# Performance work log

Measured on AMD Instinct MI355X. Metric: run time of the kernel, lower is better.

## Reference

```python
import jax, jax.numpy as jnp
import numpy as np

B, S, A = 65536, 376, 17
H1, H2, K = 400, 300, 15
MAX_ACTION = 1.0


def setup_inputs() -> dict:
    key = jax.random.key(0)
    ks = jax.random.split(key, 16)

    def lin(kw, fan_in, fan_out):
        lim = 1.0 / np.sqrt(fan_in)
        k1, k2 = jax.random.split(kw)
        W = jax.random.uniform(k1, (fan_in, fan_out), jnp.float32, -lim, lim)
        b = jax.random.uniform(k2, (fan_out,), jnp.float32, -lim, lim)
        return W, b

    W1, b1 = lin(ks[0], S, H1)
    W2, b2 = lin(ks[1], H1, H2)
    Wmu, bmu = lin(ks[2], H2, A)
    Wlv, blv = lin(ks[3], H2, A)
    Wu, bu = lin(ks[4], H2, K * A)
    Ww, bw = lin(ks[5], H2, K * A)
    Wb, bb = lin(ks[6], H2, K)
    x = jax.random.normal(ks[7], (B, S), jnp.float32)
    eps = jax.random.normal(ks[8], (B, A), jnp.float32)
    return dict(x=x, eps=eps, W1=W1, b1=b1, W2=W2, b2=b2, Wmu=Wmu, bmu=bmu,
                Wlv=Wlv, blv=blv, Wu=Wu, bu=bu, Ww=Ww, bw=bw, Wb=Wb, bb=bb)


def _flow_chain(action, u, w, b):
    # u, w: (K, B, A); b: (K, B). Sequential planar flow -> lax.scan over K.
    def step(carry, uwb):
        z, ldj = carry
        u_k, w_k, b_k = uwb
        uw = jnp.sum(w_k * u_k, -1)                       # (B,)
        m_uw = -1.0 + jax.nn.softplus(uw)
        w_norm_sq = jnp.sum(w_k * w_k, -1)
        u_hat = u_k + ((m_uw - uw) / w_norm_sq)[:, None] * w_k  # invertibility reparam
        wzb = jnp.sum(w_k * z, -1) + b_k                  # (B,)
        t = jnp.tanh(wzb)
        z_new = z + u_hat * t[:, None]
        psi_u = jnp.sum(w_k * u_hat, -1) * (1.0 - t * t)  # psi^T u_hat
        ldj_new = ldj + jnp.log(jnp.abs(1.0 + psi_u))
        return (z_new, ldj_new), None

    init = (action, jnp.zeros(action.shape[0], action.dtype))
    (z_fin, ldj), _ = jax.lax.scan(step, init, (u, w, b))
    return z_fin, ldj


def reference(x, eps, W1, b1, W2, b2, Wmu, bmu, Wlv, blv, Wu, bu, Ww, bw, Wb, bb):
    h = jax.nn.relu(x @ W1 + b1)
    h = jax.nn.relu(h @ W2 + b2)
    mu = MAX_ACTION * jnp.tanh(h @ Wmu + bmu)
    log_var = MAX_ACTION * jnp.tanh(h @ Wlv + blv)
    std = jnp.exp(log_var)                 # torch code uses log_var.exp() as the scale
    action = mu + std * eps                # rsample

    u = (h @ Wu + bu).reshape(B, K, A).transpose(1, 0, 2)   # (K, B, A)
    w = (h @ Ww + bw).reshape(B, K, A).transpose(1, 0, 2)   # (K, B, A)
    b = (h @ Wb + bb).T                                      # (K, B)

    final_action, log_det_j = _flow_chain(action, u, w, b)

    # Normal(mu, std).log_prob(action) summed over action dim; (action-mu)/std == eps
    log_2pi = jnp.float32(np.log(2.0 * np.pi))
    log_prob = jnp.sum(-0.5 * eps * eps - log_var - 0.5 * log_2pi, axis=-1)
    log_prob_final = log_prob - log_det_j
    prob_final = jnp.exp(log_prob_final)
    return final_action, prob_final, log_prob_final
```

## Files before the change

### kernel.cpp

```cpp
#include <hip/hip_runtime.h>

typedef unsigned short ushort_t;
typedef unsigned int uint_t;
typedef __bf16 bf16x8 __attribute__((ext_vector_type(8)));
typedef float f32x4 __attribute__((ext_vector_type(4)));

#define B_ROWS 65536

#define KT1 12
#define NT1 30
#define KTC1 15
#define KI2 13
#define NT2 20
#define KTC2 10
#define KI3 10
#define NT3 50
#define KTH 25


#define SZ1 (NT1 * KT1 * 512)
#define SZ2 (NT2 * KI2 * 512)
#define SZ3 (NT3 * KI3 * 512)

#define H2_US  ((size_t)4096 * KTC2 * 512)
#define HEADS_US ((size_t)4096 * KTH * 512)

__device__ inline ushort_t f2bf(float f) {
    uint_t u = __float_as_uint(f);
    return (ushort_t)((u + 0x7FFFu + ((u >> 16) & 1u)) >> 16);
}
__device__ inline uint_t pack2(float a, float b) {
    return (uint_t)f2bf(a) | ((uint_t)f2bf(b) << 16);
}
__device__ inline float fast_tanh(float x) {
    float e = __expf(2.f * x);
    return 1.f - 2.f / (e + 1.f);
}
__device__ inline void gl2lds16(const ushort_t* g, ushort_t* l) {
    __builtin_amdgcn_global_load_lds(
        (const __attribute__((address_space(1))) uint_t*)g,
        (__attribute__((address_space(3))) uint_t*)l, 16, 0, 0);
}
__device__ inline void unpack8(uint4 v, float* dst) {
    uint_t q[4] = {v.x, v.y, v.z, v.w};
    #pragma unroll
    for (int m = 0; m < 4; ++m) {
        dst[2 * m]     = __uint_as_float(q[m] << 16);
        dst[2 * m + 1] = __uint_as_float(q[m] & 0xFFFF0000u);
    }
}

__global__ void pack_kernel(const float* __restrict__ W1, const float* __restrict__ W2,
                            const float* __restrict__ Wmu, const float* __restrict__ Wlv,
                            const float* __restrict__ Wu, const float* __restrict__ Ww,
                            const float* __restrict__ Wb,
                            const float* __restrict__ b1, const float* __restrict__ b2,
                            const float* __restrict__ bmu, const float* __restrict__ blv,
                            const float* __restrict__ bu, const float* __restrict__ bw,
                            const float* __restrict__ bb,
                            ushort_t* __restrict__ W1t, ushort_t* __restrict__ W2t,
                            ushort_t* __restrict__ Wht,
                            float* __restrict__ b1p, float* __restrict__ b2p,
                            float* __restrict__ bHp)
{
    int i = blockIdx.x * 256 + threadIdx.x;
    if (i < SZ1) {
        int t = i >> 9, pos = i & 511;
        int l = pos >> 3, j = pos & 7;
        int n = (t / KT1) * 16 + (l & 15);
        int k = (t % KT1) * 32 + (l >> 4) * 8 + j;
        W1t[i] = (n < 400 && k < 376) ? f2bf(W1[k * 400 + n]) : (ushort_t)0;
    } else if (i < SZ1 + SZ2) {
        int i2 = i - SZ1;
        int t = i2 >> 9, pos = i2 & 511;
        int l = pos >> 3, j = pos & 7;
        int n = (t / KI2) * 16 + (l & 15);
        int k = (t % KI2) * 32 + (l >> 4) * 8 + j;
        W2t[i2] = (n < 300 && k < 400) ? f2bf(W2[k * 300 + n]) : (ushort_t)0;
    } else if (i < SZ1 + SZ2 + SZ3) {
        int i3 = i - SZ1 - SZ2;
        int t = i3 >> 9, pos = i3 & 511;
        int l = pos >> 3, j = pos & 7;
        int n = (t / KI3) * 16 + (l & 15);
        int k = (t % KI3) * 32 + (l >> 4) * 8 + j;
        float v = 0.f;
        if (k < 300) {
            if (n < 24)      { if (n < 17) v = Wmu[k * 17 + n]; }
            else if (n < 48) { int c = n - 24; if (c < 17) v = Wlv[k * 17 + c]; }
            else if (n < 64) { int c = n - 48; if (c < 15) v = Wb[k * 15 + c]; }
            else if (n < 784) {
                int r = n - 64, slot = r / 48, c = r % 48;
                if (c < 24) { if (c < 17) v = Wu[k * 255 + slot * 17 + c]; }
                else        { int c2 = c - 24; if (c2 < 17) v = Ww[k * 255 + slot * 17 + c2]; }
            }
        }
        Wht[i3] = f2bf(v);
    } else {
        int j = i - SZ1 - SZ2 - SZ3;
        if (j < 480) {
            b1p[j] = (j < 400) ? b1[j] : 0.f;
        } else if (j < 800) {
            int n = j - 480;
            b2p[n] = (n < 300) ? b2[n] : 0.f;
        } else if (j < 1600) {
            int n = j - 800;
            float v = 0.f;
            if (n < 24)      { if (n < 17) v = bmu[n]; }
            else if (n < 48) { int c = n - 24; if (c < 17) v = blv[c]; }
            else if (n < 64) { int c = n - 48; if (c < 15) v = bb[c]; }
            else if (n < 784) {
                int r = n - 64, slot = r / 48, c = r % 48;
                if (c < 24) { if (c < 17) v = bu[slot * 17 + c]; }
                else        { int c2 = c - 24; if (c2 < 17) v = bw[slot * 17 + c2]; }
            }
            bHp[n] = v;
        }
    }
}

template<int KITERS, int NX, bool RELU, bool CVT_A>
__global__ __launch_bounds__(256)
void gemm_db(const ushort_t* __restrict__ At, const float* __restrict__ xf,
             const ushort_t* __restrict__ Bt, const float* __restrict__ bias,
             ushort_t* __restrict__ C, int kTA, int kTC)
{
    __shared__ ushort_t As[2][8 * 512];
    __shared__ ushort_t Bs[2][10 * 512];
    const int tid = threadIdx.x;
    const int lane = tid & 63, wv = tid >> 6;
    const int q = lane >> 4, l16 = lane & 15;

    const int b = blockIdx.x;
    const int xcd = b & 7, idx = b >> 3;
    const int grp = idx / NX;
    const int bx = idx - grp * NX;
    const int by = xcd + grp * 8;
    const int nb0 = bx * 10;
    const int rowblk0 = by * 8;

    const int ct = tid >> 6;
    const int cl = tid & 63;
    const int crow0 = (rowblk0 + ct) * 16 + (cl & 15);
    const int crow1 = (rowblk0 + ct + 4) * 16 + (cl & 15);
    const int ckoff = (cl >> 4) * 8;

    f32x4 acc[2][10];
    #pragma unroll
    for (int r = 0; r < 2; ++r)
        #pragma unroll
        for (int c = 0; c < 10; ++c)
            acc[r][c] = (f32x4){0.f, 0.f, 0.f, 0.f};

    if (CVT_A) {
        #pragma unroll
        for (int j = 0; j < 2; ++j) {
            int row = j ? crow1 : crow0;
            int k0 = ckoff;
            uint4 o = {0u, 0u, 0u, 0u};
            if (k0 + 8 <= 376) {
                const float4* p = reinterpret_cast<const float4*>(
                    xf + (size_t)row * 376 + k0);
                float4 v0 = p[0], v1 = p[1];
                o.x = pack2(v0.x, v0.y); o.y = pack2(v0.z, v0.w);
                o.z = pack2(v1.x, v1.y); o.w = pack2(v1.z, v1.w);
            }
            *reinterpret_cast<uint4*>(&As[0][((ct + 4 * j) << 9) + (cl << 3)]) = o;
        }
    } else {
        #pragma unroll
        for (int i = 0; i < 2; ++i) {
            int t = wv * 2 + i;
            gl2lds16(At + (((size_t)(rowblk0 + t) * kTA + 0) << 9) + lane * 8,
                     &As[0][t << 9]);
        }
    }
    #pragma unroll
    for (int t2 = 0; t2 < 3; ++t2) {
        int t = wv + t2 * 4;
        if (t < 10)
            gl2lds16(Bt + (((size_t)(nb0 + t) * KITERS + 0) << 9) + lane * 8,
                     &Bs[0][t << 9]);
    }
    __syncthreads();

    #pragma unroll
    for (int kt = 0; kt < KITERS; ++kt) {
        const int p = kt & 1;
        uint4 nxt0, nxt1;
        if (kt + 1 < KITERS) {
            if (CVT_A) {
                int k0 = (kt + 1) * 32 + ckoff;
                nxt0 = (uint4){0u, 0u, 0u, 0u};
                nxt1 = (uint4){0u, 0u, 0u, 0u};
                if (k0 + 8 <= 376) {
                    const float4* p0 = reinterpret_cast<const float4*>(
                        xf + (size_t)crow0 * 376 + k0);
                    float4 v0 = p0[0], v1 = p0[1];
                    nxt0.x = pack2(v0.x, v0.y); nxt0.y = pack2(v0.z, v0.w);
                    nxt0.z = pack2(v1.x, v1.y); nxt0.w = pack2(v1.z, v1.w);
                    const float4* p1 = reinterpret_cast<const float4*>(
                        xf + (size_t)crow1 * 376 + k0);
                    float4 u0 = p1[0], u1 = p1[1];
                    nxt1.x = pack2(u0.x, u0.y); nxt1.y = pack2(u0.z, u0.w);
                    nxt1.z = pack2(u1.x, u1.y); nxt1.w = pack2(u1.z, u1.w);
                }
            } else {
                #pragma unroll
                for (int i = 0; i < 2; ++i) {
                    int t = wv * 2 + i;
                    gl2lds16(At + (((size_t)(rowblk0 + t) * kTA + kt + 1) << 9) + lane * 8,
                             &As[p ^ 1][t << 9]);
                }
            }
            #pragma unroll
            for (int t2 = 0; t2 < 3; ++t2) {
                int t = wv + t2 * 4;
                if (t < 10)
                    gl2lds16(Bt + (((size_t)(nb0 + t) * KITERS + kt + 1) << 9) + lane * 8,
                             &Bs[p ^ 1][t << 9]);
            }
        }

        bf16x8 a0 = __builtin_bit_cast(bf16x8,
            *reinterpret_cast<const uint4*>(&As[p][((wv * 2 + 0) << 9) + lane * 8]));
        bf16x8 a1 = __builtin_bit_cast(bf16x8,
            *reinterpret_cast<const uint4*>(&As[p][((wv * 2 + 1) << 9) + lane * 8]));
        #pragma unroll
        for (int c = 0; c < 10; ++c) {
            bf16x8 bb = __builtin_bit_cast(bf16x8,
                *reinterpret_cast<const uint4*>(&Bs[p][(c << 9) + lane * 8]));
            acc[0][c] = __builtin_amdgcn_mfma_f32_16x16x32_bf16(a0, bb, acc[0][c], 0, 0, 0);
            acc[1][c] = __builtin_amdgcn_mfma_f32_16x16x32_bf16(a1, bb, acc[1][c], 0, 0, 0);
        }

        if (CVT_A && kt + 1 < KITERS) {
            *reinterpret_cast<uint4*>(&As[p ^ 1][(ct << 9) + (cl << 3)]) = nxt0;
            *reinterpret_cast<uint4*>(&As[p ^ 1][((ct + 4) << 9) + (cl << 3)]) = nxt1;
        }
        __syncthreads();
    }

    #pragma unroll
    for (int r = 0; r < 2; ++r) {
        int rowblk = rowblk0 + wv * 2 + r;
        #pragma unroll
        for (int c = 0; c < 10; ++c) {
            int n = (nb0 + c) * 16 + l16;
            float bv = bias[n];
            #pragma unroll
            for (int reg = 0; reg < 4; ++reg) {
                float v = acc[r][c][reg] + bv;
                if (RELU) v = fmaxf(v, 0.f);
                int mrow = q * 4 + reg;
                size_t off = (((size_t)rowblk * kTC + (n >> 5)) << 9)
                           + (size_t)(((n >> 3) & 3) * 16 + mrow) * 8 + (n & 7);
                C[off] = f2bf(v);
            }
        }
    }
}

__device__ inline void ld_group8(const ushort_t* hb, int g, float* dst) {
    uint4 v = *reinterpret_cast<const uint4*>(hb + ((g >> 2) << 9) + ((g & 3) << 7));
    unpack8(v, dst);
}

__global__ __launch_bounds__(256, 4)
void flow_kernel(const ushort_t* __restrict__ heads, const float* __restrict__ eps,
                 float* __restrict__ out, int Btot)
{
    const int tid = threadIdx.x;
    const int sub = tid & 3;
    const long row = (long)blockIdx.x * 64 + (tid >> 2);
    const ushort_t* hb = heads + (((size_t)(row >> 4) * KTH) << 9)
                               + (size_t)((row & 15) << 3);

    float z[8];
    float lp = 0.f;
    {
        float amu[8] = {0,0,0,0,0,0,0,0}, alv[8] = {0,0,0,0,0,0,0,0};
        if (sub < 3) {
            ld_group8(hb, sub, amu);
            ld_group8(hb, 3 + sub, alv);
        }
        float ep[8];
        #pragma unroll
        for (int c = 0; c < 8; ++c) {
            int i = sub * 8 + c;
            ep[c] = (i < 17) ? eps[row * 17 + i] : 0.f;
        }
        #pragma unroll
        for (int c = 0; c < 8; ++c) {
            float mu = fast_tanh(amu[c]);
            float lv = fast_tanh(alv[c]);
            z[c] = mu + __expf(lv) * ep[c];
            int i = sub * 8 + c;
            lp += (i < 17) ? (-0.5f * ep[c] * ep[c] - lv - 0.918938533f) : 0.f;
        }
    }

    float bv[16];
    ld_group8(hb, 6, &bv[0]);
    ld_group8(hb, 7, &bv[8]);

    float ldj = 0.f;
    #pragma unroll
    for (int k = 0; k < 15; ++k) {
        float au[8] = {0,0,0,0,0,0,0,0}, aw[8] = {0,0,0,0,0,0,0,0};
        if (sub < 3) {
            ld_group8(hb, 8 + 6 * k + sub, au);
            ld_group8(hb, 11 + 6 * k + sub, aw);
        }
        float uw = 0.f, w2 = 0.f, wz = 0.f;
        #pragma unroll
        for (int c = 0; c < 8; ++c) {
            uw += aw[c] * au[c];
            w2 += aw[c] * aw[c];
            wz += aw[c] * z[c];
        }
        uw += __shfl_xor(uw, 1); uw += __shfl_xor(uw, 2);
        w2 += __shfl_xor(w2, 1); w2 += __shfl_xor(w2, 2);
        wz += __shfl_xor(wz, 1); wz += __shfl_xor(wz, 2);

        float sp = (uw > 15.f) ? uw : __logf(1.f + __expf(uw));
        float m = sp - 1.f;
        float coef = (m - uw) / fmaxf(w2, 1e-20f);
        float t = fast_tanh(wz + bv[k]);
        #pragma unroll
        for (int c = 0; c < 8; ++c)
            z[c] += (au[c] + coef * aw[c]) * t;
        float psi = m * (1.f - t * t);
        ldj += __logf(fmaxf(fabsf(1.f + psi), 1e-30f));
    }

    lp += __shfl_xor(lp, 1); lp += __shfl_xor(lp, 2);
    #pragma unroll
    for (int c = 0; c < 8; ++c) {
        int i = sub * 8 + c;
        if (i < 17) out[row * 17 + i] = z[c];
    }
    float lpf = lp - ldj;
    if (sub == 0) {
        out[(long)Btot * 17 + row] = __expf(lpf);
        out[(long)Btot * 18 + row] = lpf;
    }
}

extern "C" void kernel_launch(void* const* d_in, const int* in_sizes, int n_in,
                              void* d_out, int out_size, void* d_ws, size_t ws_size,
                              hipStream_t stream)
{
    const float* x   = (const float*)d_in[0];
    const float* eps = (const float*)d_in[1];
    float* out = (float*)d_out;

    ushort_t* ws = (ushort_t*)d_ws;
    ushort_t* R_h2    = ws;
    ushort_t* R_h1    = ws + H2_US;
    ushort_t* R_heads = ws + H2_US;
    ushort_t* W1t = ws + H2_US + HEADS_US;
    ushort_t* W2t = W1t + SZ1;
    ushort_t* Wht = W2t + SZ2;
    float* b1p = (float*)(Wht + SZ3);
    float* b2p = b1p + 480;
    float* bHp = b2p + 320;

    const int packN = SZ1 + SZ2 + SZ3 + 1600;
    pack_kernel<<<(packN + 255) / 256, 256, 0, stream>>>(
        (const float*)d_in[2],  (const float*)d_in[4],
        (const float*)d_in[6],  (const float*)d_in[8],
        (const float*)d_in[10], (const float*)d_in[12], (const float*)d_in[14],
        (const float*)d_in[3],  (const float*)d_in[5],
        (const float*)d_in[7],  (const float*)d_in[9],
        (const float*)d_in[11], (const float*)d_in[13], (const float*)d_in[15],
        W1t, W2t, Wht, b1p, b2p, bHp);

    gemm_db<KT1, 3, true, true><<<3 * 512, 256, 0, stream>>>(
        nullptr, x, W1t, b1p, R_h1, 0, KTC1);
    gemm_db<KI2, 2, true, false><<<2 * 512, 256, 0, stream>>>(
        R_h1, nullptr, W2t, b2p, R_h2, KTC1, KTC2);
    gemm_db<KI3, 5, false, false><<<5 * 512, 256, 0, stream>>>(
        R_h2, nullptr, Wht, bHp, R_heads, KTC2, KTH);
    flow_kernel<<<B_ROWS / 64, 256, 0, stream>>>(R_heads, eps, out, B_ROWS);
}
```

Baseline: 343.2 us.

## Keep A fragments in registers and split GEMM tiles across eight waves

The GEMM kernel now runs 512 threads, with eight waves arranged as a 4x2 grid. Each wave computes 2 row tiles by 5 column tiles instead of 2 by 10. A operands are loaded straight from global memory into registers and prefetched one k-step ahead, which drops the A shared-memory buffer. Only B stays double-buffered in LDS. This cuts the per-wave accumulator count and LDS traffic and may raise occupancy, but each A fragment is now loaded twice (once per column wave) and A reads no longer go through the async LDS path.

```diff
diff --git a/kernel.cpp b/kernel.cpp
--- a/kernel.cpp
+++ b/kernel.cpp
@@ -22,7 +22,7 @@
 #define SZ2 (NT2 * KI2 * 512)
 #define SZ3 (NT3 * KI3 * 512)
 
-#define H2_US  ((size_t)4096 * KTC2 * 512)
+#define H2_US    ((size_t)4096 * KTC2 * 512)
 #define HEADS_US ((size_t)4096 * KTH * 512)
 
 __device__ inline ushort_t f2bf(float f) {
@@ -119,15 +119,15 @@
 }
 
 template<int KITERS, int NX, bool RELU, bool CVT_A>
-__global__ __launch_bounds__(256)
-void gemm_db(const ushort_t* __restrict__ At, const float* __restrict__ xf,
+__global__ __launch_bounds__(512, 4)
+void gemm_rs(const ushort_t* __restrict__ At, const float* __restrict__ xf,
              const ushort_t* __restrict__ Bt, const float* __restrict__ bias,
              ushort_t* __restrict__ C, int kTA, int kTC)
 {
-    __shared__ ushort_t As[2][8 * 512];
     __shared__ ushort_t Bs[2][10 * 512];
     const int tid = threadIdx.x;
     const int lane = tid & 63, wv = tid >> 6;
+    const int wr = wv >> 1, wc = wv & 1;
     const int q = lane >> 4, l16 = lane & 15;
 
     const int b = blockIdx.x;
@@ -138,114 +138,73 @@
     const int nb0 = bx * 10;
     const int rowblk0 = by * 8;
 
-    const int ct = tid >> 6;
-    const int cl = tid & 63;
-    const int crow0 = (rowblk0 + ct) * 16 + (cl & 15);
-    const int crow1 = (rowblk0 + ct + 4) * 16 + (cl & 15);
-    const int ckoff = (cl >> 4) * 8;
-
-    f32x4 acc[2][10];
+    f32x4 acc[2][5];
     #pragma unroll
     for (int r = 0; r < 2; ++r)
         #pragma unroll
-        for (int c = 0; c < 10; ++c)
+        for (int c = 0; c < 5; ++c)
             acc[r][c] = (f32x4){0.f, 0.f, 0.f, 0.f};
 
-    if (CVT_A) {
-        #pragma unroll
-        for (int j = 0; j < 2; ++j) {
-            int row = j ? crow1 : crow0;
-            int k0 = ckoff;
-            uint4 o = {0u, 0u, 0u, 0u};
-            if (k0 + 8 <= 376) {
-                const float4* p = reinterpret_cast<const float4*>(
-                    xf + (size_t)row * 376 + k0);
-                float4 v0 = p[0], v1 = p[1];
-                o.x = pack2(v0.x, v0.y); o.y = pack2(v0.z, v0.w);
-                o.z = pack2(v1.x, v1.y); o.w = pack2(v1.z, v1.w);
+    auto loadA = [&](int kt, bf16x8* a) {
+        #pragma unroll
+        for (int r = 0; r < 2; ++r) {
+            int rt = rowblk0 + wr * 2 + r;
+            if (CVT_A) {
+                int row = rt * 16 + l16;
+                int k0 = kt * 32 + q * 8;
+                uint4 o = {0u, 0u, 0u, 0u};
+                if (k0 + 8 <= 376) {
+                    const float4* p = reinterpret_cast<const float4*>(
+                        xf + (size_t)row * 376 + k0);
+                    float4 v0 = p[0], v1 = p[1];
+                    o.x = pack2(v0.x, v0.y); o.y = pack2(v0.z, v0.w);
+                    o.z = pack2(v1.x, v1.y); o.w = pack2(v1.z, v1.w);
+                }
+                a[r] = __builtin_bit_cast(bf16x8, o);
+            } else {
+                a[r] = __builtin_bit_cast(bf16x8, *reinterpret_cast<const uint4*>(
+                    At + (((size_t)rt * kTA + kt) << 9) + lane * 8));
             }
-            *reinterpret_cast<uint4*>(&As[0][((ct + 4 * j) << 9) + (cl << 3)]) = o;
-        }
-    } else {
-        #pragma unroll
-        for (int i = 0; i < 2; ++i) {
-            int t = wv * 2 + i;
-            gl2lds16(At + (((size_t)(rowblk0 + t) * kTA + 0) << 9) + lane * 8,
-                     &As[0][t << 9]);
-        }
-    }
-    #pragma unroll
-    for (int t2 = 0; t2 < 3; ++t2) {
-        int t = wv + t2 * 4;
-        if (t < 10)
-            gl2lds16(Bt + (((size_t)(nb0 + t) * KITERS + 0) << 9) + lane * 8,
-                     &Bs[0][t << 9]);
-    }
+        }
+    };
+    auto stageB = [&](int kt, int buf) {
+        gl2lds16(Bt + (((size_t)(nb0 + wv) * KITERS + kt) << 9) + lane * 8,
+                 &Bs[buf][wv << 9]);
+        if (wv < 2)
+            gl2lds16(Bt + (((size_t)(nb0 + 8 + wv) * KITERS + kt) << 9) + lane * 8,
+                     &Bs[buf][(8 + wv) << 9]);
+    };
+
+    stageB(0, 0);
+    bf16x8 ac[2];
+    loadA(0, ac);
     __syncthreads();
 
     #pragma unroll
     for (int kt = 0; kt < KITERS; ++kt) {
         const int p = kt & 1;
-        uint4 nxt0, nxt1;
+        bf16x8 an[2];
         if (kt + 1 < KITERS) {
-            if (CVT_A) {
-                int k0 = (kt + 1) * 32 + ckoff;
-                nxt0 = (uint4){0u, 0u, 0u, 0u};
-                nxt1 = (uint4){0u, 0u, 0u, 0u};
-                if (k0 + 8 <= 376) {
-                    const float4* p0 = reinterpret_cast<const float4*>(
-                        xf + (size_t)crow0 * 376 + k0);
-                    float4 v0 = p0[0], v1 = p0[1];
-                    nxt0.x = pack2(v0.x, v0.y); nxt0.y = pack2(v0.z, v0.w);
-                    nxt0.z = pack2(v1.x, v1.y); nxt0.w = pack2(v1.z, v1.w);
-                    const float4* p1 = reinterpret_cast<const float4*>(
-                        xf + (size_t)crow1 * 376 + k0);
-                    float4 u0 = p1[0], u1 = p1[1];
-                    nxt1.x = pack2(u0.x, u0.y); nxt1.y = pack2(u0.z, u0.w);
-                    nxt1.z = pack2(u1.x, u1.y); nxt1.w = pack2(u1.z, u1.w);
-                }
-            } else {
-                #pragma unroll
-                for (int i = 0; i < 2; ++i) {
-                    int t = wv * 2 + i;
-                    gl2lds16(At + (((size_t)(rowblk0 + t) * kTA + kt + 1) << 9) + lane * 8,
-                             &As[p ^ 1][t << 9]);
-                }
-            }
-            #pragma unroll
-            for (int t2 = 0; t2 < 3; ++t2) {
-                int t = wv + t2 * 4;
-                if (t < 10)
-                    gl2lds16(Bt + (((size_t)(nb0 + t) * KITERS + kt + 1) << 9) + lane * 8,
-                             &Bs[p ^ 1][t << 9]);
-            }
-        }
-
-        bf16x8 a0 = __builtin_bit_cast(bf16x8,
-            *reinterpret_cast<const uint4*>(&As[p][((wv * 2 + 0) << 9) + lane * 8]));
-        bf16x8 a1 = __builtin_bit_cast(bf16x8,
-            *reinterpret_cast<const uint4*>(&As[p][((wv * 2 + 1) << 9) + lane * 8]));
-        #pragma unroll
-        for (int c = 0; c < 10; ++c) {
-            bf16x8 bb = __builtin_bit_cast(bf16x8,
-                *reinterpret_cast<const uint4*>(&Bs[p][(c << 9) + lane * 8]));
-            acc[0][c] = __builtin_amdgcn_mfma_f32_16x16x32_bf16(a0, bb, acc[0][c], 0, 0, 0);
-            acc[1][c] = __builtin_amdgcn_mfma_f32_16x16x32_bf16(a1, bb, acc[1][c], 0, 0, 0);
-        }
-
-        if (CVT_A && kt + 1 < KITERS) {
-            *reinterpret_cast<uint4*>(&As[p ^ 1][(ct << 9) + (cl << 3)]) = nxt0;
-            *reinterpret_cast<uint4*>(&As[p ^ 1][((ct + 4) << 9) + (cl << 3)]) = nxt1;
+            stageB(kt + 1, p ^ 1);
+            loadA(kt + 1, an);
+        }
+        #pragma unroll
+        for (int c = 0; c < 5; ++c) {
+            bf16x8 bb = __builtin_bit_cast(bf16x8, *reinterpret_cast<const uint4*>(
+                &Bs[p][((wc * 5 + c) << 9) + lane * 8]));
+            acc[0][c] = __builtin_amdgcn_mfma_f32_16x16x32_bf16(ac[0], bb, acc[0][c], 0, 0, 0);
+            acc[1][c] = __builtin_amdgcn_mfma_f32_16x16x32_bf16(ac[1], bb, acc[1][c], 0, 0, 0);
         }
         __syncthreads();
+        if (kt + 1 < KITERS) { ac[0] = an[0]; ac[1] = an[1]; }
     }
 
     #pragma unroll
     for (int r = 0; r < 2; ++r) {
-        int rowblk = rowblk0 + wv * 2 + r;
-        #pragma unroll
-        for (int c = 0; c < 10; ++c) {
-            int n = (nb0 + c) * 16 + l16;
+        int rowblk = rowblk0 + wr * 2 + r;
+        #pragma unroll
+        for (int c = 0; c < 5; ++c) {
+            int n = (nb0 + wc * 5 + c) * 16 + l16;
             float bv = bias[n];
             #pragma unroll
             for (int reg = 0; reg < 4; ++reg) {
@@ -375,11 +334,11 @@
         (const float*)d_in[11], (const float*)d_in[13], (const float*)d_in[15],
         W1t, W2t, Wht, b1p, b2p, bHp);
 
-    gemm_db<KT1, 3, true, true><<<3 * 512, 256, 0, stream>>>(
+    gemm_rs<KT1, 3, true, true><<<3 * 512, 512, 0, stream>>>(
         nullptr, x, W1t, b1p, R_h1, 0, KTC1);
-    gemm_db<KI2, 2, true, false><<<2 * 512, 256, 0, stream>>>(
+    gemm_rs<KI2, 2, true, false><<<2 * 512, 512, 0, stream>>>(
         R_h1, nullptr, W2t, b2p, R_h2, KTC1, KTC2);
-    gemm_db<KI3, 5, false, false><<<5 * 512, 256, 0, stream>>>(
+    gemm_rs<KI3, 5, false, false><<<5 * 512, 512, 0, stream>>>(
         R_h2, nullptr, Wht, bHp, R_heads, KTC2, KTH);
     flow_kernel<<<B_ROWS / 64, 256, 0, stream>>>(R_heads, eps, out, B_ROWS);
 }
```

After: 350.8 us. 2.2% more time.

## Fuse heads GEMM with planar flow kernel via LDS-resident head outputs

Applied to the files above, without the earlier changes.

Replaces the separate heads GEMM and flow kernel with one kernel. Each 512-thread block computes the 64x800 head outputs with MFMA, stages them in LDS as bf16, then half the threads run the 15-step planar flow on them. This removes the global write and re-read of the heads tensor and one launch. In exchange it uses about 150KB of LDS per block, which limits occupancy, and the flow phase leaves half the threads idle.

```diff
diff --git a/kernel.cpp b/kernel.cpp
--- a/kernel.cpp
+++ b/kernel.cpp
@@ -22,8 +22,8 @@
 #define SZ2 (NT2 * KI2 * 512)
 #define SZ3 (NT3 * KI3 * 512)
 
-#define H2_US  ((size_t)4096 * KTC2 * 512)
-#define HEADS_US ((size_t)4096 * KTH * 512)
+#define H2_US ((size_t)4096 * KTC2 * 512)
+#define H1_US ((size_t)4096 * KTC1 * 512)
 
 __device__ inline ushort_t f2bf(float f) {
     uint_t u = __float_as_uint(f);
@@ -260,89 +260,142 @@
     }
 }
 
-__device__ inline void ld_group8(const ushort_t* hb, int g, float* dst) {
-    uint4 v = *reinterpret_cast<const uint4*>(hb + ((g >> 2) << 9) + ((g & 3) << 7));
-    unpack8(v, dst);
-}
-
-__global__ __launch_bounds__(256, 4)
-void flow_kernel(const ushort_t* __restrict__ heads, const float* __restrict__ eps,
-                 float* __restrict__ out, int Btot)
+__global__ __launch_bounds__(512, 2)
+void gemm_flow(const ushort_t* __restrict__ At, const ushort_t* __restrict__ Bt,
+               const float* __restrict__ bias, const float* __restrict__ eps,
+               float* __restrict__ out)
 {
+    __shared__ ushort_t Bs[50 * 512];
+    __shared__ ushort_t Hd[100 * 512];
     const int tid = threadIdx.x;
-    const int sub = tid & 3;
-    const long row = (long)blockIdx.x * 64 + (tid >> 2);
-    const ushort_t* hb = heads + (((size_t)(row >> 4) * KTH) << 9)
-                               + (size_t)((row & 15) << 3);
-
-    float z[8];
-    float lp = 0.f;
-    {
-        float amu[8] = {0,0,0,0,0,0,0,0}, alv[8] = {0,0,0,0,0,0,0,0};
-        if (sub < 3) {
-            ld_group8(hb, sub, amu);
-            ld_group8(hb, 3 + sub, alv);
-        }
-        float ep[8];
+    const int lane = tid & 63, wv = tid >> 6;
+    const int wr = wv >> 1, wc = wv & 1;
+    const int q = lane >> 4, l16 = lane & 15;
+    const size_t rtg = (size_t)blockIdx.x * 4 + wr;
+    const long row0 = (long)blockIdx.x * 64;
+
+    f32x4 acc[25];
+    #pragma unroll
+    for (int c = 0; c < 25; ++c) acc[c] = (f32x4){0.f, 0.f, 0.f, 0.f};
+
+    uint4 aC = *reinterpret_cast<const uint4*>(
+        At + ((rtg * KTC2 + 0) << 9) + lane * 8);
+
+    #pragma unroll
+    for (int kt = 0; kt < KI3; ++kt) {
+        for (int t = wv; t < 50; t += 8)
+            gl2lds16(Bt + (((size_t)t * KI3 + kt) << 9) + lane * 8, &Bs[t << 9]);
+        uint4 aN;
+        if (kt + 1 < KI3)
+            aN = *reinterpret_cast<const uint4*>(
+                At + ((rtg * KTC2 + kt + 1) << 9) + lane * 8);
+        __syncthreads();
+
+        bf16x8 a = __builtin_bit_cast(bf16x8, aC);
+        #pragma unroll
+        for (int c = 0; c < 25; ++c) {
+            bf16x8 bb = __builtin_bit_cast(bf16x8, *reinterpret_cast<const uint4*>(
+                &Bs[((wc * 25 + c) << 9) + lane * 8]));
+            acc[c] = __builtin_amdgcn_mfma_f32_16x16x32_bf16(a, bb, acc[c], 0, 0, 0);
+        }
+        __syncthreads();
+        if (kt + 1 < KI3) aC = aN;
+    }
+
+    #pragma unroll
+    for (int c = 0; c < 25; ++c) {
+        int n = (wc * 25 + c) * 16 + l16;
+        float bv = bias[n];
+        #pragma unroll
+        for (int reg = 0; reg < 4; ++reg) {
+            int r16 = q * 4 + reg;
+            Hd[((wr * KTH + (n >> 5)) << 9) + (((n >> 3) & 3) << 7)
+               + (r16 << 3) + (n & 7)] = f2bf(acc[c][reg] + bv);
+        }
+    }
+    __syncthreads();
+
+    if (tid < 256) {
+        const int sub = tid & 3;
+        const int row = tid >> 2;
+        const ushort_t* hb = &Hd[(((row >> 4) * KTH) << 9) + ((row & 15) << 3)];
+        const long grow = row0 + row;
+
+        auto ldg8 = [&](int g, float* dst) {
+            uint4 v = *reinterpret_cast<const uint4*>(
+                hb + ((g >> 2) << 9) + ((g & 3) << 7));
+            unpack8(v, dst);
+        };
+
+        float z[8];
+        float lp = 0.f;
+        {
+            float amu[8] = {0,0,0,0,0,0,0,0}, alv[8] = {0,0,0,0,0,0,0,0};
+            if (sub < 3) {
+                ldg8(sub, amu);
+                ldg8(3 + sub, alv);
+            }
+            float ep[8];
+            #pragma unroll
+            for (int c = 0; c < 8; ++c) {
+                int i = sub * 8 + c;
+                ep[c] = (i < 17) ? eps[grow * 17 + i] : 0.f;
+            }
+            #pragma unroll
+            for (int c = 0; c < 8; ++c) {
+                float mu = fast_tanh(amu[c]);
+                float lv = fast_tanh(alv[c]);
+                z[c] = mu + __expf(lv) * ep[c];
+                int i = sub * 8 + c;
+                lp += (i < 17) ? (-0.5f * ep[c] * ep[c] - lv - 0.918938533f) : 0.f;
+            }
+        }
+
+        float bv[16];
+        ldg8(6, &bv[0]);
+        ldg8(7, &bv[8]);
+
+        float ldj = 0.f;
+        #pragma unroll
+        for (int k = 0; k < 15; ++k) {
+            float au[8] = {0,0,0,0,0,0,0,0}, aw[8] = {0,0,0,0,0,0,0,0};
+            if (sub < 3) {
+                ldg8(8 + 6 * k + sub, au);
+                ldg8(11 + 6 * k + sub, aw);
+            }
+            float uw = 0.f, w2 = 0.f, wz = 0.f;
+            #pragma unroll
+            for (int c = 0; c < 8; ++c) {
+                uw += aw[c] * au[c];
+                w2 += aw[c] * aw[c];
+                wz += aw[c] * z[c];
+            }
+            uw += __shfl_xor(uw, 1); uw += __shfl_xor(uw, 2);
+            w2 += __shfl_xor(w2, 1); w2 += __shfl_xor(w2, 2);
+            wz += __shfl_xor(wz, 1); wz += __shfl_xor(wz, 2);
+
+            float sp = (uw > 15.f) ? uw : __logf(1.f + __expf(uw));
+            float m = sp - 1.f;
+            float coef = (m - uw) / fmaxf(w2, 1e-20f);
+            float t = fast_tanh(wz + bv[k]);
+            #pragma unroll
+            for (int c = 0; c < 8; ++c)
+                z[c] += (au[c] + coef * aw[c]) * t;
+            float psi = m * (1.f - t * t);
+            ldj += __logf(fmaxf(fabsf(1.f + psi), 1e-30f));
+        }
+
+        lp += __shfl_xor(lp, 1); lp += __shfl_xor(lp, 2);
         #pragma unroll
         for (int c = 0; c < 8; ++c) {
             int i = sub * 8 + c;
-            ep[c] = (i < 17) ? eps[row * 17 + i] : 0.f;
-        }
-        #pragma unroll
-        for (int c = 0; c < 8; ++c) {
-            float mu = fast_tanh(amu[c]);
-            float lv = fast_tanh(alv[c]);
-            z[c] = mu + __expf(lv) * ep[c];
-            int i = sub * 8 + c;
-            lp += (i < 17) ? (-0.5f * ep[c] * ep[c] - lv - 0.918938533f) : 0.f;
-        }
-    }
-
-    float bv[16];
-    ld_group8(hb, 6, &bv[0]);
-    ld_group8(hb, 7, &bv[8]);
-
-    float ldj = 0.f;
-    #pragma unroll
-    for (int k = 0; k < 15; ++k) {
-        float au[8] = {0,0,0,0,0,0,0,0}, aw[8] = {0,0,0,0,0,0,0,0};
-        if (sub < 3) {
-            ld_group8(hb, 8 + 6 * k + sub, au);
-            ld_group8(hb, 11 + 6 * k + sub, aw);
-        }
-        float uw = 0.f, w2 = 0.f, wz = 0.f;
-        #pragma unroll
-        for (int c = 0; c < 8; ++c) {
-            uw += aw[c] * au[c];
-            w2 += aw[c] * aw[c];
-            wz += aw[c] * z[c];
-        }
-        uw += __shfl_xor(uw, 1); uw += __shfl_xor(uw, 2);
-        w2 += __shfl_xor(w2, 1); w2 += __shfl_xor(w2, 2);
-        wz += __shfl_xor(wz, 1); wz += __shfl_xor(wz, 2);
-
-        float sp = (uw > 15.f) ? uw : __logf(1.f + __expf(uw));
-        float m = sp - 1.f;
-        float coef = (m - uw) / fmaxf(w2, 1e-20f);
-        float t = fast_tanh(wz + bv[k]);
-        #pragma unroll
-        for (int c = 0; c < 8; ++c)
-            z[c] += (au[c] + coef * aw[c]) * t;
-        float psi = m * (1.f - t * t);
-        ldj += __logf(fmaxf(fabsf(1.f + psi), 1e-30f));
-    }
-
-    lp += __shfl_xor(lp, 1); lp += __shfl_xor(lp, 2);
-    #pragma unroll
-    for (int c = 0; c < 8; ++c) {
-        int i = sub * 8 + c;
-        if (i < 17) out[row * 17 + i] = z[c];
-    }
-    float lpf = lp - ldj;
-    if (sub == 0) {
-        out[(long)Btot * 17 + row] = __expf(lpf);
-        out[(long)Btot * 18 + row] = lpf;
+            if (i < 17) out[grow * 17 + i] = z[c];
+        }
+        float lpf = lp - ldj;
+        if (sub == 0) {
+            out[(long)B_ROWS * 17 + grow] = __expf(lpf);
+            out[(long)B_ROWS * 18 + grow] = lpf;
+        }
     }
 }
 
@@ -355,10 +408,9 @@
     float* out = (float*)d_out;
 
     ushort_t* ws = (ushort_t*)d_ws;
-    ushort_t* R_h2    = ws;
-    ushort_t* R_h1    = ws + H2_US;
-    ushort_t* R_heads = ws + H2_US;
-    ushort_t* W1t = ws + H2_US + HEADS_US;
+    ushort_t* R_h2 = ws;
+    ushort_t* R_h1 = ws + H2_US;
+    ushort_t* W1t = ws + H2_US + H1_US;
     ushort_t* W2t = W1t + SZ1;
     ushort_t* Wht = W2t + SZ2;
     float* b1p = (float*)(Wht + SZ3);
@@ -379,7 +431,5 @@
         nullptr, x, W1t, b1p, R_h1, 0, KTC1);
     gemm_db<KI2, 2, true, false><<<2 * 512, 256, 0, stream>>>(
         R_h1, nullptr, W2t, b2p, R_h2, KTC1, KTC2);
-    gemm_db<KI3, 5, false, false><<<5 * 512, 256, 0, stream>>>(
-        R_h2, nullptr, Wht, bHp, R_heads, KTC2, KTH);
-    flow_kernel<<<B_ROWS / 64, 256, 0, stream>>>(R_heads, eps, out, B_ROWS);
-}
+    gemm_flow<<<B_ROWS / 64, 512, 0, stream>>>(R_h2, Wht, bHp, eps, out);
+}
```

Result: no change. 349.8 us (+1.9%).

## Deepen GEMM pipeline to prefetch two k-tiles ahead with four LDS buffers

Applied to the files above, without the earlier changes.

Replaces the double-buffered GEMM loop with a four-slot LDS ring that issues loads two k-steps ahead. The fp32 x operand is held in registers and converted to bf16 one step later. Explicit vmcnt/lgkmcnt waits plus a single s_barrier per iteration replace the trailing __syncthreads. The aim is to hide global-load latency behind the MFMAs. In exchange it doubles LDS use per block, which may lower occupancy, and relies on hand-counted vmcnt values being correct.

```diff
diff --git a/kernel.cpp b/kernel.cpp
--- a/kernel.cpp
+++ b/kernel.cpp
@@ -22,7 +22,7 @@
 #define SZ2 (NT2 * KI2 * 512)
 #define SZ3 (NT3 * KI3 * 512)
 
-#define H2_US  ((size_t)4096 * KTC2 * 512)
+#define H2_US    ((size_t)4096 * KTC2 * 512)
 #define HEADS_US ((size_t)4096 * KTH * 512)
 
 __device__ inline ushort_t f2bf(float f) {
@@ -120,12 +120,12 @@
 
 template<int KITERS, int NX, bool RELU, bool CVT_A>
 __global__ __launch_bounds__(256)
-void gemm_db(const ushort_t* __restrict__ At, const float* __restrict__ xf,
+void gemm_t3(const ushort_t* __restrict__ At, const float* __restrict__ xf,
              const ushort_t* __restrict__ Bt, const float* __restrict__ bias,
              ushort_t* __restrict__ C, int kTA, int kTC)
 {
-    __shared__ ushort_t As[2][8 * 512];
-    __shared__ ushort_t Bs[2][10 * 512];
+    __shared__ ushort_t As[4][8 * 512];
+    __shared__ ushort_t Bs[4][10 * 512];
     const int tid = threadIdx.x;
     const int lane = tid & 63, wv = tid >> 6;
     const int q = lane >> 4, l16 = lane & 15;
@@ -138,12 +138,58 @@
     const int nb0 = bx * 10;
     const int rowblk0 = by * 8;
 
-    const int ct = tid >> 6;
-    const int cl = tid & 63;
+    const int ct = wv;
+    const int cl = lane;
     const int crow0 = (rowblk0 + ct) * 16 + (cl & 15);
     const int crow1 = (rowblk0 + ct + 4) * 16 + (cl & 15);
     const int ckoff = (cl >> 4) * 8;
 
+    float4 ra[2][4];
+
+    auto stage = [&](int j, int buf) {
+        if (CVT_A) {
+            int k0 = j * 32 + ckoff;
+            #pragma unroll
+            for (int r = 0; r < 2; ++r) {
+                int row = r ? crow1 : crow0;
+                float4 lo = {0.f, 0.f, 0.f, 0.f}, hi = {0.f, 0.f, 0.f, 0.f};
+                if (k0 + 8 <= 376) {
+                    const float4* p = reinterpret_cast<const float4*>(
+                        xf + (size_t)row * 376 + k0);
+                    lo = p[0]; hi = p[1];
+                }
+                ra[j & 1][2 * r] = lo;
+                ra[j & 1][2 * r + 1] = hi;
+            }
+        } else {
+            #pragma unroll
+            for (int i = 0; i < 2; ++i) {
+                int t = wv * 2 + i;
+                gl2lds16(At + (((size_t)(rowblk0 + t) * kTA + j) << 9) + lane * 8,
+                         &As[buf][t << 9]);
+            }
+        }
+        #pragma unroll
+        for (int t2 = 0; t2 < 3; ++t2) {
+            int t = wv + t2 * 4;
+            if (t < 10)
+                gl2lds16(Bt + (((size_t)(nb0 + t) * KITERS + j) << 9) + lane * 8,
+                         &Bs[buf][t << 9]);
+        }
+    };
+    auto dswriteA = [&](int j, int buf) {
+        float4 lo0 = ra[j & 1][0], hi0 = ra[j & 1][1];
+        uint4 o0;
+        o0.x = pack2(lo0.x, lo0.y); o0.y = pack2(lo0.z, lo0.w);
+        o0.z = pack2(hi0.x, hi0.y); o0.w = pack2(hi0.z, hi0.w);
+        *reinterpret_cast<uint4*>(&As[buf][(ct << 9) + (cl << 3)]) = o0;
+        float4 lo1 = ra[j & 1][2], hi1 = ra[j & 1][3];
+        uint4 o1;
+        o1.x = pack2(lo1.x, lo1.y); o1.y = pack2(lo1.z, lo1.w);
+        o1.z = pack2(hi1.x, hi1.y); o1.w = pack2(hi1.z, hi1.w);
+        *reinterpret_cast<uint4*>(&As[buf][((ct + 4) << 9) + (cl << 3)]) = o1;
+    };
+
     f32x4 acc[2][10];
     #pragma unroll
     for (int r = 0; r < 2; ++r)
@@ -151,76 +197,33 @@
         for (int c = 0; c < 10; ++c)
             acc[r][c] = (f32x4){0.f, 0.f, 0.f, 0.f};
 
-    if (CVT_A) {
-        #pragma unroll
-        for (int j = 0; j < 2; ++j) {
-            int row = j ? crow1 : crow0;
-            int k0 = ckoff;
-            uint4 o = {0u, 0u, 0u, 0u};
-            if (k0 + 8 <= 376) {
-                const float4* p = reinterpret_cast<const float4*>(
-                    xf + (size_t)row * 376 + k0);
-                float4 v0 = p[0], v1 = p[1];
-                o.x = pack2(v0.x, v0.y); o.y = pack2(v0.z, v0.w);
-                o.z = pack2(v1.x, v1.y); o.w = pack2(v1.z, v1.w);
-            }
-            *reinterpret_cast<uint4*>(&As[0][((ct + 4 * j) << 9) + (cl << 3)]) = o;
-        }
-    } else {
-        #pragma unroll
-        for (int i = 0; i < 2; ++i) {
-            int t = wv * 2 + i;
-            gl2lds16(At + (((size_t)(rowblk0 + t) * kTA + 0) << 9) + lane * 8,
-                     &As[0][t << 9]);
-        }
-    }
-    #pragma unroll
-    for (int t2 = 0; t2 < 3; ++t2) {
-        int t = wv + t2 * 4;
-        if (t < 10)
-            gl2lds16(Bt + (((size_t)(nb0 + t) * KITERS + 0) << 9) + lane * 8,
-                     &Bs[0][t << 9]);
-    }
-    __syncthreads();
+    stage(0, 0);
+    stage(1, 1);
+    if (CVT_A) dswriteA(0, 0);
 
     #pragma unroll
     for (int kt = 0; kt < KITERS; ++kt) {
-        const int p = kt & 1;
-        uint4 nxt0, nxt1;
-        if (kt + 1 < KITERS) {
-            if (CVT_A) {
-                int k0 = (kt + 1) * 32 + ckoff;
-                nxt0 = (uint4){0u, 0u, 0u, 0u};
-                nxt1 = (uint4){0u, 0u, 0u, 0u};
-                if (k0 + 8 <= 376) {
-                    const float4* p0 = reinterpret_cast<const float4*>(
-                        xf + (size_t)crow0 * 376 + k0);
-                    float4 v0 = p0[0], v1 = p0[1];
-                    nxt0.x = pack2(v0.x, v0.y); nxt0.y = pack2(v0.z, v0.w);
-                    nxt0.z = pack2(v1.x, v1.y); nxt0.w = pack2(v1.z, v1.w);
-                    const float4* p1 = reinterpret_cast<const float4*>(
-                        xf + (size_t)crow1 * 376 + k0);
-                    float4 u0 = p1[0], u1 = p1[1];
-                    nxt1.x = pack2(u0.x, u0.y); nxt1.y = pack2(u0.z, u0.w);
-                    nxt1.z = pack2(u1.x, u1.y); nxt1.w = pack2(u1.z, u1.w);
-                }
-            } else {
-                #pragma unroll
-                for (int i = 0; i < 2; ++i) {
-                    int t = wv * 2 + i;
-                    gl2lds16(At + (((size_t)(rowblk0 + t) * kTA + kt + 1) << 9) + lane * 8,
-                             &As[p ^ 1][t << 9]);
-                }
-            }
-            #pragma unroll
-            for (int t2 = 0; t2 < 3; ++t2) {
-                int t = wv + t2 * 4;
-                if (t < 10)
-                    gl2lds16(Bt + (((size_t)(nb0 + t) * KITERS + kt + 1) << 9) + lane * 8,
-                             &Bs[p ^ 1][t << 9]);
-            }
-        }
-
+        if (kt + 2 < KITERS) stage(kt + 2, (kt + 2) & 3);
+        if (CVT_A && kt + 1 < KITERS) dswriteA(kt + 1, (kt + 1) & 3);
+
+        if (CVT_A) {
+            if (kt == KITERS - 1)
+                asm volatile("s_waitcnt vmcnt(0) lgkmcnt(0)" ::: "memory");
+            else
+                asm volatile("s_waitcnt lgkmcnt(0)" ::: "memory");
+        } else {
+            if (kt + 2 < KITERS)
+                asm volatile("s_waitcnt vmcnt(8)" ::: "memory");
+            else if (kt + 1 < KITERS)
+                asm volatile("s_waitcnt vmcnt(4)" ::: "memory");
+            else
+                asm volatile("s_waitcnt vmcnt(0)" ::: "memory");
+        }
+        __builtin_amdgcn_sched_barrier(0);
+        __builtin_amdgcn_s_barrier();
+        __builtin_amdgcn_sched_barrier(0);
+
+        const int p = kt & 3;
         bf16x8 a0 = __builtin_bit_cast(bf16x8,
             *reinterpret_cast<const uint4*>(&As[p][((wv * 2 + 0) << 9) + lane * 8]));
         bf16x8 a1 = __builtin_bit_cast(bf16x8,
@@ -232,12 +235,6 @@
             acc[0][c] = __builtin_amdgcn_mfma_f32_16x16x32_bf16(a0, bb, acc[0][c], 0, 0, 0);
             acc[1][c] = __builtin_amdgcn_mfma_f32_16x16x32_bf16(a1, bb, acc[1][c], 0, 0, 0);
         }
-
-        if (CVT_A && kt + 1 < KITERS) {
-            *reinterpret_cast<uint4*>(&As[p ^ 1][(ct << 9) + (cl << 3)]) = nxt0;
-            *reinterpret_cast<uint4*>(&As[p ^ 1][((ct + 4) << 9) + (cl << 3)]) = nxt1;
-        }
-        __syncthreads();
     }
 
     #pragma unroll
@@ -375,11 +372,11 @@
         (const float*)d_in[11], (const float*)d_in[13], (const float*)d_in[15],
         W1t, W2t, Wht, b1p, b2p, bHp);
 
-    gemm_db<KT1, 3, true, true><<<3 * 512, 256, 0, stream>>>(
+    gemm_t3<KT1, 3, true, true><<<3 * 512, 256, 0, stream>>>(
         nullptr, x, W1t, b1p, R_h1, 0, KTC1);
-    gemm_db<KI2, 2, true, false><<<2 * 512, 256, 0, stream>>>(
+    gemm_t3<KI2, 2, true, false><<<2 * 512, 256, 0, stream>>>(
         R_h1, nullptr, W2t, b2p, R_h2, KTC1, KTC2);
-    gemm_db<KI3, 5, false, false><<<5 * 512, 256, 0, stream>>>(
+    gemm_t3<KI3, 5, false, false><<<5 * 512, 256, 0, stream>>>(
         R_h2, nullptr, Wht, bHp, R_heads, KTC2, KTH);
     flow_kernel<<<B_ROWS / 64, 256, 0, stream>>>(R_heads, eps, out, B_ROWS);
 }
```

After: 330.6 us. -3.7%, faster.
